# Kernel tuning notes

Measured on AMD Instinct MI355X. Metric: run time of the kernel, lower is better.

## Reference

```python
import jax, jax.numpy as jnp
import numpy as np

N = 100000   # nodes
E = 1600000  # edges
G = 2048     # graphs in batch
NF = 64      # node_feature_dim
D = 32       # hidden dim (hard-coded in module)
SF = 512     # solvent_feature_dim
BN_EPS = 1e-5


def setup_inputs() -> dict:
    key = jax.random.key(0)
    ks = jax.random.split(key, 24)
    s = 0.1
    return {
        "x": jax.random.normal(ks[0], (N, NF), jnp.float32),
        "edge_index": jax.random.randint(ks[1], (2, E), 0, N, dtype=jnp.int64),
        "batch": jnp.sort(jax.random.randint(ks[2], (N,), 0, G, dtype=jnp.int64)),
        "solvent_fingerprint": jax.random.uniform(ks[3], (G, SF), jnp.float32),
        # GIN layer 1 first Linear (NF->D); layers 2-5 first Linear stacked (D->D)
        "w1a": jax.random.normal(ks[4], (NF, D), jnp.float32) * s,
        "b1a": jnp.zeros((D,), jnp.float32),
        "ws_a": jax.random.normal(ks[5], (4, D, D), jnp.float32) * s,
        "bs_a": jnp.zeros((4, D), jnp.float32),
        # second Linear of all 5 GIN MLPs
        "ws_b": jax.random.normal(ks[6], (5, D, D), jnp.float32) * s,
        "bs_b": jnp.zeros((5, D), jnp.float32),
        # BatchNorm affine params per layer
        "bn_g": jnp.ones((5, D), jnp.float32),
        "bn_b": jnp.zeros((5, D), jnp.float32),
        # dense head
        "fcg_w": jax.random.normal(ks[7], (D, 128), jnp.float32) * s,
        "fcg_b": jnp.zeros((128,), jnp.float32),
        "fs1_w": jax.random.normal(ks[8], (SF, 256), jnp.float32) * s,
        "fs1_b": jnp.zeros((256,), jnp.float32),
        "fs2_w": jax.random.normal(ks[9], (256, 128), jnp.float32) * s,
        "fs2_b": jnp.zeros((128,), jnp.float32),
        "fc1_w": jax.random.normal(ks[10], (256, 1024), jnp.float32) * s,
        "fc1_b": jnp.zeros((1024,), jnp.float32),
        "fc2_w": jax.random.normal(ks[11], (1024, 256), jnp.float32) * s,
        "fc2_b": jnp.zeros((256,), jnp.float32),
        "out_w": jax.random.normal(ks[12], (256, 1), jnp.float32) * s,
        "out_b": jnp.zeros((1,), jnp.float32),
    }


def _bn_relu(h, g, b):
    # BatchNorm1d training-mode math (biased batch variance), then ReLU
    mu = h.mean(axis=0)
    var = h.var(axis=0)
    return jax.nn.relu((h - mu) * jax.lax.rsqrt(var + BN_EPS) * g + b)


def reference(x, edge_index, batch, solvent_fingerprint,
              w1a, b1a, ws_a, bs_a, ws_b, bs_b, bn_g, bn_b,
              fcg_w, fcg_b, fs1_w, fs1_b, fs2_w, fs2_b,
              fc1_w, fc1_b, fc2_w, fc2_b, out_w, out_b):
    src, dst = edge_index[0], edge_index[1]

    def gin_agg(h):
        # GINConv with eps=0: (1+eps)*x_i + sum_{j->i} x_j
        return h + jax.ops.segment_sum(h[src], dst, num_segments=N)

    # layer 1 (NF -> D)
    h = gin_agg(x)
    h = jax.nn.relu(h @ w1a + b1a) @ ws_b[0] + bs_b[0]
    h = _bn_relu(h, bn_g[0], bn_b[0])
    # layers 2-5 (D -> D)
    for i in range(4):
        h = gin_agg(h)
        h = jax.nn.relu(h @ ws_a[i] + bs_a[i]) @ ws_b[i + 1] + bs_b[i + 1]
        h = _bn_relu(h, bn_g[i + 1], bn_b[i + 1])

    pooled = jax.ops.segment_sum(h, batch, num_segments=G)  # [G, D]
    gfeat = jax.nn.relu(pooled @ fcg_w + fcg_b)             # dropout inactive (eval)

    sf = solvent_fingerprint.reshape(-1, SF)
    s = jax.nn.relu(sf @ fs1_w + fs1_b)
    s = jax.nn.relu(s @ fs2_w + fs2_b)

    z = jnp.concatenate([gfeat, s], axis=1)                 # [G, 256]
    z = jax.nn.relu(z @ fc1_w + fc1_b)
    z = jax.nn.relu(z @ fc2_w + fc2_b)
    return z @ out_w + out_b                                # [G, 1]
```

## Files before the change

kernel.cpp:

```cpp
#include <hip/hip_runtime.h>
#include <hip/hip_bf16.h>

static constexpr int N_NODES = 100000;
static constexpr int N_EDGES = 1600000;
static constexpr int N_GRAPH = 2048;
static constexpr float BN_EPS_C = 1e-5f;

static constexpr int BUCK_SHIFT = 9;
static constexpr int NB_BUCK = (N_NODES + 511) >> 9;
static constexpr int PART_B = 256;
static constexpr int CHUNK = N_EDGES / PART_B;
static constexpr int NTOT = NB_BUCK * PART_B;

typedef unsigned int uint;
typedef unsigned short ushort;


__device__ inline uint pk2(float a, float b) {
    uint ua = __float_as_uint(a), ub = __float_as_uint(b);
    ua = (ua + 0x7fffu + ((ua >> 16) & 1u)) >> 16;
    ub = (ub + 0x7fffu + ((ub >> 16) & 1u)) >> 16;
    return ua | (ub << 16);
}
__device__ inline float b2f_lo(uint u) { return __uint_as_float(u << 16); }
__device__ inline float b2f_hi(uint u) { return __uint_as_float(u & 0xffff0000u); }

__device__ inline void unpack8(uint4 v, float* f) {
    f[0] = b2f_lo(v.x); f[1] = b2f_hi(v.x);
    f[2] = b2f_lo(v.y); f[3] = b2f_hi(v.y);
    f[4] = b2f_lo(v.z); f[5] = b2f_hi(v.z);
    f[6] = b2f_lo(v.w); f[7] = b2f_hi(v.w);
}


__global__ __launch_bounds__(256) void k_bcount(const int* __restrict__ dst, int* __restrict__ cnt) {
    __shared__ int h[NB_BUCK];
    int blk = blockIdx.x, tid = threadIdx.x;
    for (int i = tid; i < NB_BUCK; i += 256) h[i] = 0;
    __syncthreads();
    int base = blk * CHUNK;
    for (int e = base + tid; e < base + CHUNK; e += 256) {
        int d = __builtin_nontemporal_load(&dst[e]);
        atomicAdd(&h[d >> BUCK_SHIFT], 1);
    }
    __syncthreads();
    for (int i = tid; i < NB_BUCK; i += 256) cnt[i * PART_B + blk] = h[i];
}

__global__ __launch_bounds__(256) void k_scan_partial2(const int* __restrict__ v, int* __restrict__ part, int n) {
    __shared__ int sw[4];
    int b = blockIdx.x, tid = threadIdx.x;
    int base = b * 1024;
    int s = 0;
#pragma unroll
    for (int r = 0; r < 4; ++r) {
        int i = base + r * 256 + tid;
        if (i < n) s += v[i];
    }
#pragma unroll
    for (int off = 32; off > 0; off >>= 1) s += __shfl_down(s, off);
    if ((tid & 63) == 0) sw[tid >> 6] = s;
    __syncthreads();
    if (tid == 0) part[b] = sw[0] + sw[1] + sw[2] + sw[3];
}

__global__ __launch_bounds__(256) void k_scan_offsets2(int* __restrict__ part, int nb, int* __restrict__ bstart) {
    __shared__ int sh[256];
    int tid = threadIdx.x;
    sh[tid] = (tid < nb) ? part[tid] : 0;
    __syncthreads();
    if (tid == 0) {
        int run = 0;
        for (int i = 0; i < nb; ++i) { int v = sh[i]; sh[i] = run; run += v; }
        bstart[NB_BUCK] = run;
    }
    __syncthreads();
    if (tid < nb) part[tid] = sh[tid];
}

__global__ __launch_bounds__(256) void k_scan_final2(int* __restrict__ cnt, const int* __restrict__ part,
                                                     int* __restrict__ bstart, int n) {
    __shared__ int wsum[4];
    int b = blockIdx.x, tid = threadIdx.x;
    int lane = tid & 63, w = tid >> 6;
    int base = b * 1024 + tid * 4;
    int v[4];
#pragma unroll
    for (int r = 0; r < 4; ++r) {
        int i = base + r;
        v[r] = (i < n) ? cnt[i] : 0;
    }
    int tsum = v[0] + v[1] + v[2] + v[3];
    int inc = tsum;
#pragma unroll
    for (int off = 1; off < 64; off <<= 1) {
        int t = __shfl_up(inc, off);
        if (lane >= off) inc += t;
    }
    if (lane == 63) wsum[w] = inc;
    __syncthreads();
    int woff = 0;
    for (int ww = 0; ww < w; ++ww) woff += wsum[ww];
    int run = part[b] + woff + (inc - tsum);
#pragma unroll
    for (int r = 0; r < 4; ++r) {
        int idx = base + r;
        if (idx < n) {
            int c = v[r];
            cnt[idx] = run;
            if ((idx & (PART_B - 1)) == 0) bstart[idx / PART_B] = run;
            run += c;
        }
    }
}

__global__ __launch_bounds__(256) void k_bpart(const int* __restrict__ src, const int* __restrict__ dst,
                                               const int* __restrict__ cnt, int2* __restrict__ ebuf) {
    __shared__ int cur[NB_BUCK];
    int blk = blockIdx.x, tid = threadIdx.x;
    for (int i = tid; i < NB_BUCK; i += 256) cur[i] = cnt[i * PART_B + blk];
    __syncthreads();
    int base = blk * CHUNK;
    for (int e = base + tid; e < base + CHUNK; e += 256) {
        int d = __builtin_nontemporal_load(&dst[e]);
        int s = __builtin_nontemporal_load(&src[e]);
        int p = atomicAdd(&cur[d >> BUCK_SHIFT], 1);
        ebuf[p] = make_int2(d, s);
    }
}

__global__ __launch_bounds__(256) void k_bfine(const int2* __restrict__ ebuf, const int* __restrict__ bstart,
                                               int* __restrict__ row_ptr, int* __restrict__ row_end,
                                               int* __restrict__ ssrc) {
    __shared__ int fh[512];
    __shared__ int wsum[4];
    int b = blockIdx.x, tid = threadIdx.x;
    int n0 = b << BUCK_SHIFT;
    int e0 = bstart[b], e1 = bstart[b + 1];
    fh[tid] = 0; fh[tid + 256] = 0;
    __syncthreads();
    for (int e = e0 + tid; e < e1; e += 256)
        atomicAdd(&fh[ebuf[e].x - n0], 1);
    __syncthreads();
    int a0 = fh[2 * tid], a1 = fh[2 * tid + 1];
    int s = a0 + a1;
    int lane = tid & 63, w = tid >> 6;
    int inc = s;
#pragma unroll
    for (int off = 1; off < 64; off <<= 1) {
        int t = __shfl_up(inc, off);
        if (lane >= off) inc += t;
    }
    if (lane == 63) wsum[w] = inc;
    __syncthreads();
    int woff = 0;
    for (int ww = 0; ww < w; ++ww) woff += wsum[ww];
    int excl = woff + inc - s;
    int p0 = excl, p1 = excl + a0;
    int node0 = n0 + 2 * tid, node1 = node0 + 1;
    if (node0 < N_NODES) { row_ptr[node0] = e0 + p0; row_end[node0] = e0 + p0 + a0; }
    if (node1 < N_NODES) { row_ptr[node1] = e0 + p1; row_end[node1] = e0 + p1 + a1; }
    fh[2 * tid] = p0; fh[2 * tid + 1] = p1;
    __syncthreads();
    for (int e = e0 + tid; e < e1; e += 256) {
        int2 v = ebuf[e];
        int p = atomicAdd(&fh[v.x - n0], 1);
        ssrc[e0 + p] = v.y;
    }
}


__global__ __launch_bounds__(256) void k_gather64b(const ushort* __restrict__ xb,
                                                   const int* __restrict__ row_ptr, const int* __restrict__ row_end,
                                                   const int* __restrict__ ssrc, float* __restrict__ out) {
    int idx = blockIdx.x * 256 + threadIdx.x;
    int node = idx >> 3;
    if (node >= N_NODES) return;
    int f8 = (idx & 7) * 8;
    float acc[8];
    unpack8(*(const uint4*)(xb + (size_t)node * 64 + f8), acc);
    int e = row_ptr[node], e1 = row_end[node];
    for (; e + 2 <= e1; e += 2) {
        int s0 = ssrc[e], s1 = ssrc[e + 1];
        uint4 va = *(const uint4*)(xb + (size_t)s0 * 64 + f8);
        uint4 vb = *(const uint4*)(xb + (size_t)s1 * 64 + f8);
        float v[8];
        unpack8(va, v);
#pragma unroll
        for (int j = 0; j < 8; ++j) acc[j] += v[j];
        unpack8(vb, v);
#pragma unroll
        for (int j = 0; j < 8; ++j) acc[j] += v[j];
    }
    if (e < e1) {
        int s = ssrc[e];
        float v[8];
        unpack8(*(const uint4*)(xb + (size_t)s * 64 + f8), v);
#pragma unroll
        for (int j = 0; j < 8; ++j) acc[j] += v[j];
    }
    float* op = out + (size_t)node * 64 + f8;
    *(float4*)op = make_float4(acc[0], acc[1], acc[2], acc[3]);
    *(float4*)(op + 4) = make_float4(acc[4], acc[5], acc[6], acc[7]);
}

__global__ __launch_bounds__(256) void k_gather64(const float* __restrict__ x,
                                                  const int* __restrict__ row_ptr, const int* __restrict__ row_end,
                                                  const int* __restrict__ ssrc, float* __restrict__ out) {
    int idx = blockIdx.x * 256 + threadIdx.x;
    int node = idx >> 4;
    if (node >= N_NODES) return;
    int f = (idx & 15) * 4;
    float4 acc = *(const float4*)(x + (size_t)node * 64 + f);
    int e1 = row_end[node];
    for (int e = row_ptr[node]; e < e1; ++e) {
        int s = ssrc[e];
        float4 v = *(const float4*)(x + (size_t)s * 64 + f);
        acc.x += v.x; acc.y += v.y; acc.z += v.z; acc.w += v.w;
    }
    *(float4*)(out + (size_t)node * 64 + f) = acc;
}

__global__ __launch_bounds__(256) void k_gather_bn_b(const ushort* __restrict__ u, const float* __restrict__ stats,
                                                     const float* __restrict__ bng, const float* __restrict__ bnb,
                                                     const int* __restrict__ row_ptr, const int* __restrict__ row_end,
                                                     const int* __restrict__ ssrc, float* __restrict__ out) {
    int idx = blockIdx.x * 256 + threadIdx.x;
    int node = idx >> 2;
    if (node >= N_NODES) return;
    int f8 = (idx & 3) * 8;
    const float inv = 1.0f / (float)N_NODES;
    float sc[8], sh[8];
    {
        float s1[8], s2[8], g[8], b[8];
        *(float4*)s1 = *(const float4*)(stats + f8);       *(float4*)(s1 + 4) = *(const float4*)(stats + f8 + 4);
        *(float4*)s2 = *(const float4*)(stats + 32 + f8);  *(float4*)(s2 + 4) = *(const float4*)(stats + 36 + f8);
        *(float4*)g  = *(const float4*)(bng + f8);         *(float4*)(g + 4)  = *(const float4*)(bng + f8 + 4);
        *(float4*)b  = *(const float4*)(bnb + f8);         *(float4*)(b + 4)  = *(const float4*)(bnb + f8 + 4);
#pragma unroll
        for (int j = 0; j < 8; ++j) {
            float mu = s1[j] * inv;
            sc[j] = rsqrtf(s2[j] * inv - mu * mu + BN_EPS_C) * g[j];
            sh[j] = b[j] - mu * sc[j];
        }
    }
    float acc[8], v[8];
    unpack8(*(const uint4*)(u + (size_t)node * 32 + f8), v);
#pragma unroll
    for (int j = 0; j < 8; ++j) acc[j] = fmaxf(fmaf(v[j], sc[j], sh[j]), 0.f);
    int e = row_ptr[node], e1 = row_end[node];
    for (; e + 2 <= e1; e += 2) {
        int s0 = ssrc[e], s1 = ssrc[e + 1];
        uint4 va = *(const uint4*)(u + (size_t)s0 * 32 + f8);
        uint4 vb = *(const uint4*)(u + (size_t)s1 * 32 + f8);
        unpack8(va, v);
#pragma unroll
        for (int j = 0; j < 8; ++j) acc[j] += fmaxf(fmaf(v[j], sc[j], sh[j]), 0.f);
        unpack8(vb, v);
#pragma unroll
        for (int j = 0; j < 8; ++j) acc[j] += fmaxf(fmaf(v[j], sc[j], sh[j]), 0.f);
    }
    if (e < e1) {
        int s = ssrc[e];
        unpack8(*(const uint4*)(u + (size_t)s * 32 + f8), v);
#pragma unroll
        for (int j = 0; j < 8; ++j) acc[j] += fmaxf(fmaf(v[j], sc[j], sh[j]), 0.f);
    }
    float* op = out + (size_t)node * 32 + f8;
    *(float4*)op = make_float4(acc[0], acc[1], acc[2], acc[3]);
    *(float4*)(op + 4) = make_float4(acc[4], acc[5], acc[6], acc[7]);
}


template <int K>
__global__ __launch_bounds__(256) void k_mlp_stats(const float* __restrict__ agg,
                                                   const float* __restrict__ Wa, const float* __restrict__ ba,
                                                   const float* __restrict__ Wb, const float* __restrict__ bb,
                                                   ushort* __restrict__ u, float* __restrict__ stats) {
    __shared__ float sWa[K * 32];
    __shared__ float sWb[1024];
    __shared__ float sba[32];
    __shared__ float sbb[32];
    __shared__ float tile[256][33];
    __shared__ float bstats[64];
    int tid = threadIdx.x;
    for (int i = tid; i < K * 32; i += 256) sWa[i] = Wa[i];
    for (int i = tid; i < 1024; i += 256) sWb[i] = Wb[i];
    if (tid < 32) { sba[tid] = ba[tid]; sbb[tid] = bb[tid]; }
    if (tid < 64) bstats[tid] = 0.f;
    __syncthreads();
    int node = blockIdx.x * 256 + tid;
    bool active = node < N_NODES;

    {
        float t[32];
#pragma unroll
        for (int j = 0; j < 32; ++j) t[j] = sba[j];
        if (active) {
            const float* arow = agg + (size_t)node * K;
            for (int k = 0; k < K; k += 4) {
                float4 a4 = *(const float4*)(arow + k);
                float av[4] = {a4.x, a4.y, a4.z, a4.w};
#pragma unroll
                for (int kk = 0; kk < 4; ++kk) {
                    float a = av[kk];
                    const float4* wr = (const float4*)(sWa + (k + kk) * 32);
#pragma unroll
                    for (int j4 = 0; j4 < 8; ++j4) {
                        float4 wv = wr[j4];
                        t[j4 * 4 + 0] = fmaf(a, wv.x, t[j4 * 4 + 0]);
                        t[j4 * 4 + 1] = fmaf(a, wv.y, t[j4 * 4 + 1]);
                        t[j4 * 4 + 2] = fmaf(a, wv.z, t[j4 * 4 + 2]);
                        t[j4 * 4 + 3] = fmaf(a, wv.w, t[j4 * 4 + 3]);
                    }
                }
            }
        }
#pragma unroll
        for (int j = 0; j < 32; ++j) tile[tid][j] = fmaxf(t[j], 0.f);
    }
    __syncthreads();

    float uu[32];
#pragma unroll
    for (int j = 0; j < 32; ++j) uu[j] = sbb[j];
#pragma unroll 4
    for (int k = 0; k < 32; ++k) {
        float a = tile[tid][k];
        const float4* wr = (const float4*)(sWb + k * 32);
#pragma unroll
        for (int j4 = 0; j4 < 8; ++j4) {
            float4 wv = wr[j4];
            uu[j4 * 4 + 0] = fmaf(a, wv.x, uu[j4 * 4 + 0]);
            uu[j4 * 4 + 1] = fmaf(a, wv.y, uu[j4 * 4 + 1]);
            uu[j4 * 4 + 2] = fmaf(a, wv.z, uu[j4 * 4 + 2]);
            uu[j4 * 4 + 3] = fmaf(a, wv.w, uu[j4 * 4 + 3]);
        }
    }
    if (active) {
        uint pk[16];
#pragma unroll
        for (int j = 0; j < 16; ++j) pk[j] = pk2(uu[2 * j], uu[2 * j + 1]);
        uint4* up = (uint4*)(u + (size_t)node * 32);
        up[0] = make_uint4(pk[0], pk[1], pk[2], pk[3]);
        up[1] = make_uint4(pk[4], pk[5], pk[6], pk[7]);
        up[2] = make_uint4(pk[8], pk[9], pk[10], pk[11]);
        up[3] = make_uint4(pk[12], pk[13], pk[14], pk[15]);
    } else {
#pragma unroll
        for (int j = 0; j < 32; ++j) uu[j] = 0.f;
    }

#pragma unroll
    for (int j = 0; j < 32; ++j) {
        float v = uu[j];
        float v2 = v * v;
#pragma unroll
        for (int off = 32; off > 0; off >>= 1) {
            v += __shfl_down(v, off);
            v2 += __shfl_down(v2, off);
        }
        if ((tid & 63) == 0) {
            atomicAdd(&bstats[j], v);
            atomicAdd(&bstats[32 + j], v2);
        }
    }
    __syncthreads();
    if (tid < 64) atomicAdd(&stats[tid], bstats[tid]);
}


__global__ __launch_bounds__(256) void k_bn_pool(const ushort* __restrict__ u, const float* __restrict__ stats,
                                                 const float* __restrict__ bng, const float* __restrict__ bnb,
                                                 const int* __restrict__ batch, float* __restrict__ pooled) {
    const int CH = 128;
    int wid = (blockIdx.x * 256 + threadIdx.x) >> 6;
    int lane = threadIdx.x & 63;
    int f = lane & 31, par = lane >> 5;
    int n0 = wid * CH;
    if (n0 >= N_NODES) return;
    int n1 = n0 + CH; if (n1 > N_NODES) n1 = N_NODES;
    const float inv = 1.0f / (float)N_NODES;
    float mu = stats[f] * inv;
    float var = stats[32 + f] * inv - mu * mu;
    float sc = rsqrtf(var + BN_EPS_C) * bng[f];
    float sh = bnb[f] - mu * sc;
    float acc = 0.f;
    int curg = -1;
    for (int n = n0 + par; n < n1; n += 2) {
        int g = batch[n];
        if (g != curg) {
            if (curg >= 0) atomicAdd(&pooled[(size_t)curg * 32 + f], acc);
            acc = 0.f; curg = g;
        }
        float v = b2f_lo((uint)u[(size_t)n * 32 + f]);
        acc += fmaxf(fmaf(v, sc, sh), 0.f);
    }
    if (curg >= 0) atomicAdd(&pooled[(size_t)curg * 32 + f], acc);
}


__global__ __launch_bounds__(256) void k_cvt_bf16(const float* __restrict__ x, ushort* __restrict__ xb, int n) {
    int i = (blockIdx.x * 256 + threadIdx.x) * 8;
    if (i >= n) return;
    float4 a = *(const float4*)(x + i);
    float4 b = *(const float4*)(x + i + 4);
    *(uint4*)(xb + i) = make_uint4(pk2(a.x, a.y), pk2(a.z, a.w), pk2(b.x, b.y), pk2(b.z, b.w));
}


#define GEMM_COMPUTE_16()                                                      \
    _Pragma("unroll")                                                          \
    for (int k = 0; k < 16; ++k) {                                             \
        float4 a4 = *(const float4*)&As[k][ty * 4];                            \
        float4 b4 = *(const float4*)&Bs[k][tx * 4];                            \
        acc[0][0] = fmaf(a4.x, b4.x, acc[0][0]);                               \
        acc[0][1] = fmaf(a4.x, b4.y, acc[0][1]);                               \
        acc[0][2] = fmaf(a4.x, b4.z, acc[0][2]);                               \
        acc[0][3] = fmaf(a4.x, b4.w, acc[0][3]);                               \
        acc[1][0] = fmaf(a4.y, b4.x, acc[1][0]);                               \
        acc[1][1] = fmaf(a4.y, b4.y, acc[1][1]);                               \
        acc[1][2] = fmaf(a4.y, b4.z, acc[1][2]);                               \
        acc[1][3] = fmaf(a4.y, b4.w, acc[1][3]);                               \
        acc[2][0] = fmaf(a4.z, b4.x, acc[2][0]);                               \
        acc[2][1] = fmaf(a4.z, b4.y, acc[2][1]);                               \
        acc[2][2] = fmaf(a4.z, b4.z, acc[2][2]);                               \
        acc[2][3] = fmaf(a4.z, b4.w, acc[2][3]);                               \
        acc[3][0] = fmaf(a4.w, b4.x, acc[3][0]);                               \
        acc[3][1] = fmaf(a4.w, b4.y, acc[3][1]);                               \
        acc[3][2] = fmaf(a4.w, b4.z, acc[3][2]);                               \
        acc[3][3] = fmaf(a4.w, b4.w, acc[3][3]);                               \
    }

__global__ __launch_bounds__(256) void k_gemm_f(const float* __restrict__ A, const float* __restrict__ B,
                                                const float* __restrict__ bias, float* __restrict__ C,
                                                int Nc, int K, int ldc, int do_relu) {
    __shared__ float As[16][64];
    __shared__ float Bs[16][64];
    int tid = threadIdx.x;
    int tx = tid & 15, ty = tid >> 4;
    int bm = blockIdx.x * 64, bn = blockIdx.y * 64;
    float acc[4][4] = {{0.f}};
    int am = tid >> 2;
    int ak = (tid & 3) * 4;
    int bk = tid >> 4;
    int bn4 = (tid & 15) * 4;
    const float* Ap = A + (size_t)(bm + am) * K + ak;
    const float* Bp = B + (size_t)bk * Nc + bn + bn4;
    float4 av = *(const float4*)Ap;
    float4 bv = *(const float4*)Bp;
    for (int k0 = 0; k0 < K; k0 += 16) {
        As[ak + 0][am] = av.x;
        As[ak + 1][am] = av.y;
        As[ak + 2][am] = av.z;
        As[ak + 3][am] = av.w;
        *(float4*)&Bs[bk][bn4] = bv;
        __syncthreads();
        if (k0 + 16 < K) {
            av = *(const float4*)(Ap + k0 + 16);
            bv = *(const float4*)(Bp + (size_t)(k0 + 16) * Nc);
        }
        GEMM_COMPUTE_16()
        __syncthreads();
    }
    float4 bi = *(const float4*)(bias + bn + tx * 4);
#pragma unroll
    for (int i = 0; i < 4; ++i) {
        float4 v;
        v.x = acc[i][0] + bi.x;
        v.y = acc[i][1] + bi.y;
        v.z = acc[i][2] + bi.z;
        v.w = acc[i][3] + bi.w;
        if (do_relu) {
            v.x = fmaxf(v.x, 0.f); v.y = fmaxf(v.y, 0.f);
            v.z = fmaxf(v.z, 0.f); v.w = fmaxf(v.w, 0.f);
        }
        *(float4*)(C + (size_t)(bm + ty * 4 + i) * ldc + bn + tx * 4) = v;
    }
}

__global__ __launch_bounds__(256) void k_gemm_p(const float* __restrict__ A, const float* __restrict__ B,
                                                float* __restrict__ psum, int Nc, int Ktot, int klen) {
    __shared__ float As[16][64];
    __shared__ float Bs[16][64];
    int tid = threadIdx.x;
    int tx = tid & 15, ty = tid >> 4;
    int bm = blockIdx.x * 64, bn = blockIdx.y * 64;
    int kb = blockIdx.z * klen;
    float acc[4][4] = {{0.f}};
    int am = tid >> 2;
    int ak = (tid & 3) * 4;
    int bk = tid >> 4;
    int bn4 = (tid & 15) * 4;
    const float* Ap = A + (size_t)(bm + am) * Ktot + kb + ak;
    const float* Bp = B + (size_t)(kb + bk) * Nc + bn + bn4;
    float4 av = *(const float4*)Ap;
    float4 bv = *(const float4*)Bp;
    for (int k0 = 0; k0 < klen; k0 += 16) {
        As[ak + 0][am] = av.x;
        As[ak + 1][am] = av.y;
        As[ak + 2][am] = av.z;
        As[ak + 3][am] = av.w;
        *(float4*)&Bs[bk][bn4] = bv;
        __syncthreads();
        if (k0 + 16 < klen) {
            av = *(const float4*)(Ap + k0 + 16);
            bv = *(const float4*)(Bp + (size_t)(k0 + 16) * Nc);
        }
        GEMM_COMPUTE_16()
        __syncthreads();
    }
    float* out = psum + (size_t)blockIdx.z * N_GRAPH * Nc;
#pragma unroll
    for (int i = 0; i < 4; ++i) {
        float4 v = make_float4(acc[i][0], acc[i][1], acc[i][2], acc[i][3]);
        *(float4*)(out + (size_t)(bm + ty * 4 + i) * Nc + bn + tx * 4) = v;
    }
}

__global__ __launch_bounds__(256) void k_reduce(const float* __restrict__ psum, const float* __restrict__ bias,
                                                float* __restrict__ C, int S, int Nc, int ldc, int do_relu) {
    int idx = blockIdx.x * 256 + threadIdx.x;
    int nq = Nc >> 2;
    if (idx >= N_GRAPH * nq) return;
    int m = idx / nq;
    int j = (idx - m * nq) * 4;
    float4 s = *(const float4*)(psum + (size_t)m * Nc + j);
    for (int z = 1; z < S; ++z) {
        float4 t = *(const float4*)(psum + (size_t)z * N_GRAPH * Nc + (size_t)m * Nc + j);
        s.x += t.x; s.y += t.y; s.z += t.z; s.w += t.w;
    }
    float4 bi = *(const float4*)(bias + j);
    s.x += bi.x; s.y += bi.y; s.z += bi.z; s.w += bi.w;
    if (do_relu) {
        s.x = fmaxf(s.x, 0.f); s.y = fmaxf(s.y, 0.f);
        s.z = fmaxf(s.z, 0.f); s.w = fmaxf(s.w, 0.f);
    }
    *(float4*)(C + (size_t)m * ldc + j) = s;
}


__global__ __launch_bounds__(256) void k_out(const float* __restrict__ z2, const float* __restrict__ w,
                                             const float* __restrict__ b, float* __restrict__ out) {
    int gid = blockIdx.x * 256 + threadIdx.x;
    int g = gid >> 6;
    int lane = threadIdx.x & 63;
    if (g >= N_GRAPH) return;
    float4 a = *(const float4*)(z2 + (size_t)g * 256 + lane * 4);
    float4 wv = *(const float4*)(w + lane * 4);
    float v = a.x * wv.x + a.y * wv.y + a.z * wv.z + a.w * wv.w;
#pragma unroll
    for (int off = 32; off > 0; off >>= 1) v += __shfl_down(v, off);
    if (lane == 0) out[g] = v + b[0];
}


extern "C" void kernel_launch(void* const* d_in, const int* in_sizes, int n_in,
                              void* d_out, int out_size, void* d_ws, size_t ws_size,
                              hipStream_t stream) {
    const float* x     = (const float*)d_in[0];
    const int*   eidx  = (const int*)d_in[1];
    const int*   batch = (const int*)d_in[2];
    const float* sf    = (const float*)d_in[3];
    const float* w1a   = (const float*)d_in[4];
    const float* b1a   = (const float*)d_in[5];
    const float* ws_a  = (const float*)d_in[6];
    const float* bs_a  = (const float*)d_in[7];
    const float* ws_b  = (const float*)d_in[8];
    const float* bs_b  = (const float*)d_in[9];
    const float* bn_g  = (const float*)d_in[10];
    const float* bn_b  = (const float*)d_in[11];
    const float* fcg_w = (const float*)d_in[12];
    const float* fcg_b = (const float*)d_in[13];
    const float* fs1_w = (const float*)d_in[14];
    const float* fs1_b = (const float*)d_in[15];
    const float* fs2_w = (const float*)d_in[16];
    const float* fs2_b = (const float*)d_in[17];
    const float* fc1_w = (const float*)d_in[18];
    const float* fc1_b = (const float*)d_in[19];
    const float* fc2_w = (const float*)d_in[20];
    const float* fc2_b = (const float*)d_in[21];
    const float* out_w = (const float*)d_in[22];
    const float* out_b = (const float*)d_in[23];
    float* dout = (float*)d_out;

    char* p = (char*)d_ws;
    float*  agg     = (float*)p;  p += (size_t)N_NODES * 64 * 4;
    ushort* ubuf    = (ushort*)p; p += (size_t)N_NODES * 32 * 2;
    int*    ssrc    = (int*)p;    p += (size_t)N_EDGES * 4;
    int*    row_ptr = (int*)p;    p += (size_t)N_NODES * 4;
    int*    row_end = (int*)p;    p += (size_t)N_NODES * 4;
    int*    cnt     = (int*)p;    p += (size_t)NTOT * 4;
    int*    part2   = (int*)p;    p += 512 * 4;
    int*    bstart  = (int*)p;    p += 256 * 4;
    float*  stats   = (float*)p;  p += 320 * 4;
    float*  pooled  = (float*)p;  p += (size_t)N_GRAPH * 32 * 4;
    ushort* xb      = (ushort*)p; p += (size_t)N_NODES * 64 * 2;
    bool use_xb = ((size_t)(p - (char*)d_ws) <= ws_size);

    int2* ebuf = (int2*)agg;

    float* zcat  = agg;
    float* z1buf = zcat + 2048 * 256;
    float* z2buf = z1buf + 2048 * 1024;
    float* s1buf = z2buf + 2048 * 256;
    float* psum  = s1buf + 2048 * 256;

    size_t zero_bytes = (320 + (size_t)N_GRAPH * 32) * 4;
    hipMemsetAsync(stats, 0, zero_bytes, stream);

    const int* esrc = eidx;
    const int* edst = eidx + N_EDGES;

    const int scan_blocks = NTOT / 1024;
    k_bcount<<<PART_B, 256, 0, stream>>>(edst, cnt);
    k_scan_partial2<<<scan_blocks, 256, 0, stream>>>(cnt, part2, NTOT);
    k_scan_offsets2<<<1, 256, 0, stream>>>(part2, scan_blocks, bstart);
    k_scan_final2<<<scan_blocks, 256, 0, stream>>>(cnt, part2, bstart, NTOT);
    k_bpart<<<PART_B, 256, 0, stream>>>(esrc, edst, cnt, ebuf);
    k_bfine<<<NB_BUCK, 256, 0, stream>>>(ebuf, bstart, row_ptr, row_end, ssrc);

    if (use_xb) {
        k_cvt_bf16<<<(N_NODES * 64 / 8 + 255) / 256, 256, 0, stream>>>(x, xb, N_NODES * 64);
        k_gather64b<<<(N_NODES * 8) / 256, 256, 0, stream>>>(xb, row_ptr, row_end, ssrc, agg);
    } else {
        k_gather64<<<(N_NODES * 16) / 256, 256, 0, stream>>>(x, row_ptr, row_end, ssrc, agg);
    }
    k_mlp_stats<64><<<(N_NODES + 255) / 256, 256, 0, stream>>>(agg, w1a, b1a, ws_b, bs_b, ubuf, stats);
    for (int L = 1; L <= 4; ++L) {
        k_gather_bn_b<<<(N_NODES * 4 + 255) / 256, 256, 0, stream>>>(
            ubuf, stats + (L - 1) * 64, bn_g + (L - 1) * 32, bn_b + (L - 1) * 32,
            row_ptr, row_end, ssrc, agg);
        k_mlp_stats<32><<<(N_NODES + 255) / 256, 256, 0, stream>>>(
            agg, ws_a + (size_t)(L - 1) * 1024, bs_a + (L - 1) * 32,
            ws_b + (size_t)L * 1024, bs_b + L * 32, ubuf, stats + L * 64);
    }
    {
        int waves = (N_NODES + 127) / 128;
        int blocks = (waves + 3) / 4;
        k_bn_pool<<<blocks, 256, 0, stream>>>(ubuf, stats + 256, bn_g + 128, bn_b + 128, batch, pooled);
    }

    k_gemm_f<<<dim3(32, 2), 256, 0, stream>>>(pooled, fcg_w, fcg_b, zcat, 128, 32, 256, 1);
    k_gemm_p<<<dim3(32, 4, 4), 256, 0, stream>>>(sf, fs1_w, psum, 256, 512, 128);
    k_reduce<<<512, 256, 0, stream>>>(psum, fs1_b, s1buf, 4, 256, 256, 1);
    k_gemm_p<<<dim3(32, 2, 4), 256, 0, stream>>>(s1buf, fs2_w, psum, 128, 256, 64);
    k_reduce<<<256, 256, 0, stream>>>(psum, fs2_b, zcat + 128, 4, 128, 256, 1);
    k_gemm_f<<<dim3(32, 16), 256, 0, stream>>>(zcat, fc1_w, fc1_b, z1buf, 1024, 256, 1024, 1);
    k_gemm_p<<<dim3(32, 4, 4), 256, 0, stream>>>(z1buf, fc2_w, psum, 256, 1024, 256);
    k_reduce<<<512, 256, 0, stream>>>(psum, fc2_b, z2buf, 4, 256, 256, 1);
    k_out<<<512, 256, 0, stream>>>(z2buf, out_w, out_b, dout);
}
```

Baseline: 589.1 us.

## Read MLP weights from global memory, tile-based BN stats, and spread stat atomics over slots

The MLP+stats kernel no longer stages weights and biases in shared memory. It reads them straight from global memory with uniform indices, which the compiler can turn into scalar loads, and keeps the hidden activations in registers instead of a shared tile. The per-feature wave-shuffle reduction is replaced by writing outputs to a shared tile and summing columns with 128 threads. The final global atomics are spread over 8 stat slots, which consumers add back together. This aims to cut shared-memory traffic, barriers, shuffle chains and atomic contention, at the cost of extra register pressure and a small per-thread slot summation in the gather and pool kernels.

```diff
diff --git a/kernel.cpp b/kernel.cpp
--- a/kernel.cpp
+++ b/kernel.cpp
@@ -11,6 +11,7 @@
 static constexpr int PART_B = 256;
 static constexpr int CHUNK = N_EDGES / PART_B;
 static constexpr int NTOT = NB_BUCK * PART_B;
+static constexpr int NSLOT = 8;
 
 typedef unsigned int uint;
 typedef unsigned short ushort;
@@ -232,11 +233,21 @@
     const float inv = 1.0f / (float)N_NODES;
     float sc[8], sh[8];
     {
-        float s1[8], s2[8], g[8], b[8];
-        *(float4*)s1 = *(const float4*)(stats + f8);       *(float4*)(s1 + 4) = *(const float4*)(stats + f8 + 4);
-        *(float4*)s2 = *(const float4*)(stats + 32 + f8);  *(float4*)(s2 + 4) = *(const float4*)(stats + 36 + f8);
-        *(float4*)g  = *(const float4*)(bng + f8);         *(float4*)(g + 4)  = *(const float4*)(bng + f8 + 4);
-        *(float4*)b  = *(const float4*)(bnb + f8);         *(float4*)(b + 4)  = *(const float4*)(bnb + f8 + 4);
+        float s1[8] = {0,0,0,0,0,0,0,0}, s2[8] = {0,0,0,0,0,0,0,0};
+        for (int s = 0; s < NSLOT; ++s) {
+            const float* sp = stats + s * 64;
+            float4 a = *(const float4*)(sp + f8);
+            float4 b = *(const float4*)(sp + f8 + 4);
+            float4 c = *(const float4*)(sp + 32 + f8);
+            float4 d = *(const float4*)(sp + 36 + f8);
+            s1[0] += a.x; s1[1] += a.y; s1[2] += a.z; s1[3] += a.w;
+            s1[4] += b.x; s1[5] += b.y; s1[6] += b.z; s1[7] += b.w;
+            s2[0] += c.x; s2[1] += c.y; s2[2] += c.z; s2[3] += c.w;
+            s2[4] += d.x; s2[5] += d.y; s2[6] += d.z; s2[7] += d.w;
+        }
+        float g[8], b[8];
+        *(float4*)g = *(const float4*)(bng + f8); *(float4*)(g + 4) = *(const float4*)(bng + f8 + 4);
+        *(float4*)b = *(const float4*)(bnb + f8); *(float4*)(b + 4) = *(const float4*)(bnb + f8 + 4);
 #pragma unroll
         for (int j = 0; j < 8; ++j) {
             float mu = s1[j] * inv;
@@ -277,66 +288,44 @@
                                                    const float* __restrict__ Wa, const float* __restrict__ ba,
                                                    const float* __restrict__ Wb, const float* __restrict__ bb,
                                                    ushort* __restrict__ u, float* __restrict__ stats) {
-    __shared__ float sWa[K * 32];
-    __shared__ float sWb[1024];
-    __shared__ float sba[32];
-    __shared__ float sbb[32];
-    __shared__ float tile[256][33];
+    __shared__ float tile[256][36];
     __shared__ float bstats[64];
     int tid = threadIdx.x;
-    for (int i = tid; i < K * 32; i += 256) sWa[i] = Wa[i];
-    for (int i = tid; i < 1024; i += 256) sWb[i] = Wb[i];
-    if (tid < 32) { sba[tid] = ba[tid]; sbb[tid] = bb[tid]; }
     if (tid < 64) bstats[tid] = 0.f;
-    __syncthreads();
     int node = blockIdx.x * 256 + tid;
     bool active = node < N_NODES;
 
-    {
-        float t[32];
-#pragma unroll
-        for (int j = 0; j < 32; ++j) t[j] = sba[j];
-        if (active) {
-            const float* arow = agg + (size_t)node * K;
-            for (int k = 0; k < K; k += 4) {
-                float4 a4 = *(const float4*)(arow + k);
-                float av[4] = {a4.x, a4.y, a4.z, a4.w};
-#pragma unroll
-                for (int kk = 0; kk < 4; ++kk) {
-                    float a = av[kk];
-                    const float4* wr = (const float4*)(sWa + (k + kk) * 32);
-#pragma unroll
-                    for (int j4 = 0; j4 < 8; ++j4) {
-                        float4 wv = wr[j4];
-                        t[j4 * 4 + 0] = fmaf(a, wv.x, t[j4 * 4 + 0]);
-                        t[j4 * 4 + 1] = fmaf(a, wv.y, t[j4 * 4 + 1]);
-                        t[j4 * 4 + 2] = fmaf(a, wv.z, t[j4 * 4 + 2]);
-                        t[j4 * 4 + 3] = fmaf(a, wv.w, t[j4 * 4 + 3]);
-                    }
-                }
+    float h[32];
+#pragma unroll
+    for (int j = 0; j < 32; ++j) h[j] = ba[j];
+    if (active) {
+        const float* arow = agg + (size_t)node * K;
+        for (int k = 0; k < K; k += 4) {
+            float4 a4 = *(const float4*)(arow + k);
+            float av[4] = {a4.x, a4.y, a4.z, a4.w};
+#pragma unroll
+            for (int kk = 0; kk < 4; ++kk) {
+                float a = av[kk];
+                const float* wr = Wa + (k + kk) * 32;
+#pragma unroll
+                for (int j = 0; j < 32; ++j) h[j] = fmaf(a, wr[j], h[j]);
             }
         }
-#pragma unroll
-        for (int j = 0; j < 32; ++j) tile[tid][j] = fmaxf(t[j], 0.f);
-    }
-    __syncthreads();
+    }
+#pragma unroll
+    for (int j = 0; j < 32; ++j) h[j] = fmaxf(h[j], 0.f);
 
     float uu[32];
 #pragma unroll
-    for (int j = 0; j < 32; ++j) uu[j] = sbb[j];
-#pragma unroll 4
+    for (int j = 0; j < 32; ++j) uu[j] = bb[j];
+#pragma unroll
     for (int k = 0; k < 32; ++k) {
-        float a = tile[tid][k];
-        const float4* wr = (const float4*)(sWb + k * 32);
-#pragma unroll
-        for (int j4 = 0; j4 < 8; ++j4) {
-            float4 wv = wr[j4];
-            uu[j4 * 4 + 0] = fmaf(a, wv.x, uu[j4 * 4 + 0]);
-            uu[j4 * 4 + 1] = fmaf(a, wv.y, uu[j4 * 4 + 1]);
-            uu[j4 * 4 + 2] = fmaf(a, wv.z, uu[j4 * 4 + 2]);
-            uu[j4 * 4 + 3] = fmaf(a, wv.w, uu[j4 * 4 + 3]);
-        }
-    }
+        float a = h[k];
+        const float* wr = Wb + k * 32;
+#pragma unroll
+        for (int j = 0; j < 32; ++j) uu[j] = fmaf(a, wr[j], uu[j]);
+    }
+
     if (active) {
         uint pk[16];
 #pragma unroll
@@ -352,21 +341,23 @@
     }
 
 #pragma unroll
-    for (int j = 0; j < 32; ++j) {
-        float v = uu[j];
-        float v2 = v * v;
-#pragma unroll
-        for (int off = 32; off > 0; off >>= 1) {
-            v += __shfl_down(v, off);
-            v2 += __shfl_down(v2, off);
-        }
-        if ((tid & 63) == 0) {
-            atomicAdd(&bstats[j], v);
-            atomicAdd(&bstats[32 + j], v2);
-        }
-    }
-    __syncthreads();
-    if (tid < 64) atomicAdd(&stats[tid], bstats[tid]);
+    for (int q = 0; q < 8; ++q)
+        *(float4*)&tile[tid][q * 4] = make_float4(uu[q * 4], uu[q * 4 + 1], uu[q * 4 + 2], uu[q * 4 + 3]);
+    __syncthreads();
+    if (tid < 128) {
+        int w = tid >> 5, j = tid & 31;
+        int r0 = w * 64;
+        float sv = 0.f, sv2 = 0.f;
+        for (int r = 0; r < 64; ++r) {
+            float v = tile[r0 + r][j];
+            sv += v;
+            sv2 = fmaf(v, v, sv2);
+        }
+        atomicAdd(&bstats[j], sv);
+        atomicAdd(&bstats[32 + j], sv2);
+    }
+    __syncthreads();
+    if (tid < 64) atomicAdd(&stats[(blockIdx.x & (NSLOT - 1)) * 64 + tid], bstats[tid]);
 }
 
 
@@ -381,8 +372,10 @@
     if (n0 >= N_NODES) return;
     int n1 = n0 + CH; if (n1 > N_NODES) n1 = N_NODES;
     const float inv = 1.0f / (float)N_NODES;
-    float mu = stats[f] * inv;
-    float var = stats[32 + f] * inv - mu * mu;
+    float sv = 0.f, sq = 0.f;
+    for (int s = 0; s < NSLOT; ++s) { sv += stats[s * 64 + f]; sq += stats[s * 64 + 32 + f]; }
+    float mu = sv * inv;
+    float var = sq * inv - mu * mu;
     float sc = rsqrtf(var + BN_EPS_C) * bng[f];
     float sh = bnb[f] - mu * sc;
     float acc = 0.f;
@@ -593,7 +586,7 @@
     int*    cnt     = (int*)p;    p += (size_t)NTOT * 4;
     int*    part2   = (int*)p;    p += 512 * 4;
     int*    bstart  = (int*)p;    p += 256 * 4;
-    float*  stats   = (float*)p;  p += 320 * 4;
+    float*  stats   = (float*)p;  p += (size_t)5 * NSLOT * 64 * 4;
     float*  pooled  = (float*)p;  p += (size_t)N_GRAPH * 32 * 4;
     ushort* xb      = (ushort*)p; p += (size_t)N_NODES * 64 * 2;
     bool use_xb = ((size_t)(p - (char*)d_ws) <= ws_size);
@@ -606,7 +599,7 @@
     float* s1buf = z2buf + 2048 * 256;
     float* psum  = s1buf + 2048 * 256;
 
-    size_t zero_bytes = (320 + (size_t)N_GRAPH * 32) * 4;
+    size_t zero_bytes = ((size_t)5 * NSLOT * 64 + (size_t)N_GRAPH * 32) * 4;
     hipMemsetAsync(stats, 0, zero_bytes, stream);
 
     const int* esrc = eidx;
@@ -620,25 +613,29 @@
     k_bpart<<<PART_B, 256, 0, stream>>>(esrc, edst, cnt, ebuf);
     k_bfine<<<NB_BUCK, 256, 0, stream>>>(ebuf, bstart, row_ptr, row_end, ssrc);
 
+    const int mlp_blocks = (N_NODES + 255) / 256;
+    const int SLOT_STRIDE = NSLOT * 64;
+
     if (use_xb) {
         k_cvt_bf16<<<(N_NODES * 64 / 8 + 255) / 256, 256, 0, stream>>>(x, xb, N_NODES * 64);
         k_gather64b<<<(N_NODES * 8) / 256, 256, 0, stream>>>(xb, row_ptr, row_end, ssrc, agg);
     } else {
         k_gather64<<<(N_NODES * 16) / 256, 256, 0, stream>>>(x, row_ptr, row_end, ssrc, agg);
     }
-    k_mlp_stats<64><<<(N_NODES + 255) / 256, 256, 0, stream>>>(agg, w1a, b1a, ws_b, bs_b, ubuf, stats);
+    k_mlp_stats<64><<<mlp_blocks, 256, 0, stream>>>(agg, w1a, b1a, ws_b, bs_b, ubuf, stats);
     for (int L = 1; L <= 4; ++L) {
         k_gather_bn_b<<<(N_NODES * 4 + 255) / 256, 256, 0, stream>>>(
-            ubuf, stats + (L - 1) * 64, bn_g + (L - 1) * 32, bn_b + (L - 1) * 32,
+            ubuf, stats + (size_t)(L - 1) * SLOT_STRIDE, bn_g + (L - 1) * 32, bn_b + (L - 1) * 32,
             row_ptr, row_end, ssrc, agg);
-        k_mlp_stats<32><<<(N_NODES + 255) / 256, 256, 0, stream>>>(
+        k_mlp_stats<32><<<mlp_blocks, 256, 0, stream>>>(
             agg, ws_a + (size_t)(L - 1) * 1024, bs_a + (L - 1) * 32,
-            ws_b + (size_t)L * 1024, bs_b + L * 32, ubuf, stats + L * 64);
+            ws_b + (size_t)L * 1024, bs_b + L * 32, ubuf, stats + (size_t)L * SLOT_STRIDE);
     }
     {
         int waves = (N_NODES + 127) / 128;
         int blocks = (waves + 3) / 4;
-        k_bn_pool<<<blocks, 256, 0, stream>>>(ubuf, stats + 256, bn_g + 128, bn_b + 128, batch, pooled);
+        k_bn_pool<<<blocks, 256, 0, stream>>>(ubuf, stats + (size_t)4 * SLOT_STRIDE,
+                                              bn_g + 128, bn_b + 128, batch, pooled);
     }
 
     k_gemm_f<<<dim3(32, 2), 256, 0, stream>>>(pooled, fcg_w, fcg_b, zcat, 128, 32, 256, 1);
```

Measured after the change: 602.8 us. +2.3%, slower.
